# Kernel optimization log

Hardware: AMD Instinct MI355X
Metric: run time of the kernel (lower is better)

The kernel has to match this reference:

```python
import jax, jax.numpy as jnp
import numpy as np

B, NQ, NKV, DQ, DIN = 8, 2048, 2048, 512, 512


def setup_inputs() -> dict:
    key = jax.random.key(0)
    ks = jax.random.split(key, 5)
    scale = 1.0 / np.sqrt(DQ)
    return {
        "query": jax.random.normal(ks[0], (B, NQ, DQ), dtype=jnp.float32),
        "key": jax.random.normal(ks[1], (NKV, DQ), dtype=jnp.float32),
        "x": jax.random.normal(ks[2], (B, NKV, DIN), dtype=jnp.float32),
        "W_proj": jax.random.normal(ks[3], (DQ, DQ), dtype=jnp.float32) * scale,
        "b_proj": jnp.zeros((DQ,), dtype=jnp.float32),
        "W_px": jax.random.normal(ks[4], (DQ, DIN), dtype=jnp.float32) * scale,
        "b_px": jnp.zeros((DQ,), dtype=jnp.float32),
    }


def reference(query, key, x, W_proj, b_proj, W_px, b_px):
    # query_proj = Linear(dim_query, dim_query)(query)            [B, Nq, DQ]
    query_proj = jnp.einsum("bqd,ed->bqe", query, W_proj) + b_proj
    # k = project_x(x) + key.unsqueeze(0)                          [B, Nkv, DQ]
    k = jnp.einsum("bki,ei->bke", x, W_px) + b_px + key[None, :, :]
    # score = bmm(query_proj, k^T)                                 [B, Nq, Nkv]
    score = jnp.einsum("bqe,bke->bqk", query_proj, k)
    # softmax=True branch (note: original applies NO 1/sqrt(d) scaling)
    attn = jax.nn.softmax(score, axis=-1)
    # out = bmm(attn, x)                                           [B, Nq, DIN]
    out = jnp.einsum("bqk,bki->bqi", attn, x)
    return out, attn
```

## Files before the change

kernel.cpp:

```cpp
#include <hip/hip_runtime.h>
#include <hip/hip_bf16.h>

#define B_   8
#define NQ_  2048
#define NKV_ 2048
#define DQ_  512
#define DIN_ 512

using f32x4 = __attribute__((ext_vector_type(4))) float;
using f16   = _Float16;
using f16x4 = __attribute__((ext_vector_type(4))) _Float16;
using f16x8 = __attribute__((ext_vector_type(8))) _Float16;

__device__ __forceinline__ f32x4 mfma16f(f16x8 a, f16x8 b, f32x4 c) {
  return __builtin_amdgcn_mfma_f32_16x16x32_f16(a, b, c, 0, 0, 0);
}

__device__ __forceinline__ void gload_lds16(const void* g, void* l) {
  __builtin_amdgcn_global_load_lds(
      (const __attribute__((address_space(1))) void*)g,
      (__attribute__((address_space(3))) void*)l, 16, 0, 0);
}

__device__ __forceinline__ int xcd_swz(int bid, int nwg) {
  const int c = nwg >> 3;
  return (bid & 7) * c + (bid >> 3);
}

__global__ __launch_bounds__(256, 2)
void proj_gemm(const float* __restrict__ query, const float* __restrict__ W_proj,
               const float* __restrict__ b_proj, f16* __restrict__ qp,
               const float* __restrict__ x, const float* __restrict__ W_px,
               const float* __restrict__ b_px, const float* __restrict__ keyp,
               f16* __restrict__ km, f16* __restrict__ xTp)
{
  constexpr int PAD = 8;
  __shared__ f16 Ah[128][64 + PAD];
  __shared__ f16 Bh[128][64 + PAD];

  const bool second = (blockIdx.z == 1);
  const float* A    = second ? x    : query;
  const float* Bm   = second ? W_px : W_proj;
  const float* bias = second ? b_px : b_proj;
  f16*         C    = second ? km   : qp;

  const int tid  = threadIdx.x;
  const int lane = tid & 63;
  const int w    = tid >> 6;
  const int wr   = w >> 1;
  const int wc   = w & 1;
  const int brow = blockIdx.y * 128;
  const int bcol = blockIdx.x * 128;

  const float* Ag = A  + (size_t)brow * DQ_;
  const float* Bg = Bm + (size_t)bcol * DQ_;

  f32x4 acc[4][4] = {};

  const int sr = tid >> 4;
  const int sc = (tid & 15) * 4;

  float4 pa[8], pb[8];
#pragma unroll
  for (int p = 0; p < 8; ++p) {
    pa[p] = *(const float4*)(Ag + (size_t)(p * 16 + sr) * DQ_ + sc);
    pb[p] = *(const float4*)(Bg + (size_t)(p * 16 + sr) * DQ_ + sc);
  }

  const bool emitXT = second && (blockIdx.x == 0);

  for (int k0 = 0; k0 < DQ_; k0 += 64) {
    __syncthreads();
#pragma unroll
    for (int p = 0; p < 8; ++p) {
      const int r = p * 16 + sr;
      f16x4 ha, hb;
      ha[0] = (f16)pa[p].x; ha[1] = (f16)pa[p].y;
      ha[2] = (f16)pa[p].z; ha[3] = (f16)pa[p].w;
      hb[0] = (f16)pb[p].x; hb[1] = (f16)pb[p].y;
      hb[2] = (f16)pb[p].z; hb[3] = (f16)pb[p].w;
      *(f16x4*)&Ah[r][sc] = ha;
      *(f16x4*)&Bh[r][sc] = hb;
    }
    if (k0 + 64 < DQ_) {
#pragma unroll
      for (int p = 0; p < 8; ++p) {
        pa[p] = *(const float4*)(Ag + (size_t)(p * 16 + sr) * DQ_ + k0 + 64 + sc);
        pb[p] = *(const float4*)(Bg + (size_t)(p * 16 + sr) * DQ_ + k0 + 64 + sc);
      }
    }
    __syncthreads();
#pragma unroll
    for (int kk = 0; kk < 2; ++kk) {
      const int fr = lane & 15;
      const int fc = kk * 32 + (lane >> 4) * 8;
      f16x8 ah[4], bh[4];
#pragma unroll
      for (int m = 0; m < 4; ++m)
        ah[m] = *(const f16x8*)&Ah[wr * 64 + m * 16 + fr][fc];
#pragma unroll
      for (int n = 0; n < 4; ++n)
        bh[n] = *(const f16x8*)&Bh[wc * 64 + n * 16 + fr][fc];
#pragma unroll
      for (int m = 0; m < 4; ++m)
#pragma unroll
        for (int n = 0; n < 4; ++n)
          acc[m][n] = mfma16f(ah[m], bh[n], acc[m][n]);
    }

    if (emitXT) {
      const int dl = tid >> 2;
      const int j0 = (tid & 3) * 32;
      f16* dst = xTp + ((size_t)(brow >> 11) * DIN_ + k0 + dl) * NKV_
                     + (brow & (NKV_ - 1)) + j0;
#pragma unroll
      for (int v = 0; v < 4; ++v) {
        f16x8 tv;
#pragma unroll
        for (int e = 0; e < 8; ++e) tv[e] = Ah[j0 + v * 8 + e][dl];
        *(f16x8*)(dst + v * 8) = tv;
      }
    }
  }

#pragma unroll
  for (int m = 0; m < 4; ++m)
#pragma unroll
    for (int n = 0; n < 4; ++n)
#pragma unroll
      for (int r = 0; r < 4; ++r) {
        const int row_g = brow + wr * 64 + m * 16 + (lane >> 4) * 4 + r;
        const int col_g = bcol + wc * 64 + n * 16 + (lane & 15);
        float vv = acc[m][n][r] + bias[col_g];
        if (second) vv += keyp[(size_t)(row_g & (NKV_ - 1)) * DQ_ + col_g];
        C[(size_t)row_g * DQ_ + col_g] = (f16)vv;
      }
}

__global__ __launch_bounds__(512, 2)
void score_gemm(const f16* __restrict__ qp, const f16* __restrict__ km,
                float* __restrict__ attn)
{
  __shared__ f16 ABuf[2 * 8192];
  __shared__ f16 BBuf[2 * 8192];

  const int swz  = xcd_swz(blockIdx.x, gridDim.x);
  const int bx   = swz & 7;
  const int by   = (swz >> 3) & 7;
  const int b    = swz >> 6;

  const int t    = threadIdx.x;
  const int lane = t & 63;
  const int w    = t >> 6;
  const int wr   = w >> 2;
  const int wcn  = w & 3;
  const int brow = by * 256;
  const int bcol = bx * 256;
  const int fr   = lane & 15;
  const int q    = lane >> 4;
  const int slotE = ((q ^ (fr & 3)) * 8);

  const int srow = t >> 2;
  const int sig  = (t & 3) ^ (srow & 3);
  const f16* aG = qp + ((size_t)b * NQ_  + brow + srow) * DQ_ + sig * 8;
  const f16* bG = km + ((size_t)b * NKV_ + bcol + srow) * DQ_ + sig * 8;

#define STAGE_A(kc) do { \
    const f16* s_ = aG + (kc) * 32; \
    f16* d_ = ABuf + ((kc) & 1) * 8192 + w * 512; \
    gload_lds16(s_, d_); \
    gload_lds16(s_ + (size_t)128 * DQ_, d_ + 4096); } while (0)
#define STAGE_B(kc) do { \
    const f16* s_ = bG + (kc) * 32; \
    f16* d_ = BBuf + ((kc) & 1) * 8192 + w * 512; \
    gload_lds16(s_, d_); \
    gload_lds16(s_ + (size_t)128 * DQ_, d_ + 4096); } while (0)

  f32x4 acc[8][4] = {};

  STAGE_A(0); STAGE_B(0);
  asm volatile("s_waitcnt vmcnt(0)\n\ts_barrier" ::: "memory");

  for (int c = 0; c < 16; ++c) {
    if (c + 1 < 16) { STAGE_A(c + 1); STAGE_B(c + 1); }

    const f16* Ab = ABuf + (c & 1) * 8192;
    const f16* Bb = BBuf + (c & 1) * 8192;

    f16x8 bh[4];
#pragma unroll
    for (int ni = 0; ni < 4; ++ni)
      bh[ni] = *(const f16x8*)&Bb[(wcn * 64 + ni * 16 + fr) * 32 + slotE];

    __builtin_amdgcn_s_setprio(1);
#pragma unroll
    for (int mi = 0; mi < 8; ++mi) {
      const f16x8 ah = *(const f16x8*)&Ab[(wr * 128 + mi * 16 + fr) * 32 + slotE];
#pragma unroll
      for (int ni = 0; ni < 4; ++ni)
        acc[mi][ni] = mfma16f(ah, bh[ni], acc[mi][ni]);
    }
    __builtin_amdgcn_s_setprio(0);

    if (c + 1 < 16)
      asm volatile("s_waitcnt vmcnt(0)\n\ts_barrier" ::: "memory");
  }
#undef STAGE_A
#undef STAGE_B

  float* Cg = attn + (size_t)b * NQ_ * NKV_;
#pragma unroll
  for (int mi = 0; mi < 8; ++mi)
#pragma unroll
    for (int ni = 0; ni < 4; ++ni)
#pragma unroll
      for (int r = 0; r < 4; ++r) {
        const int row_g = brow + wr * 128 + mi * 16 + q * 4 + r;
        const int col_g = bcol + wcn * 64 + ni * 16 + fr;
        Cg[(size_t)row_g * NKV_ + col_g] = acc[mi][ni][r];
      }
}

__global__ __launch_bounds__(256, 2)
void pv_gemm(const f16* __restrict__ attnb, const f16* __restrict__ xT,
             float* __restrict__ out)
{
  __shared__ f16 At[2][128 * 64];
  __shared__ f16 Bt[2][128 * 64];

  const int swz  = xcd_swz(blockIdx.x, gridDim.x);
  const int bx   = swz & 3;
  const int by   = (swz >> 2) & 15;
  const int b    = swz >> 6;

  const int t    = threadIdx.x;
  const int lane = t & 63;
  const int w    = t >> 6;
  const int wr   = w >> 1;
  const int wc   = w & 1;
  const int brow = by * 128;
  const int bcol = bx * 128;

  const int srow  = t >> 3;
  const int sslot = t & 7;
  const int sig   = sslot ^ (srow & 7);
  const f16* aG = attnb + ((size_t)b * NQ_ + brow + srow) * NKV_ + sig * 8;
  const f16* bG = xT + (size_t)b * DIN_ * NKV_ + (size_t)(bcol + srow) * NKV_ + sig * 8;

  f32x4 acc[4][4] = {};
  const int fr = lane & 15;
  const int q  = lane >> 4;

#define PV_STAGE(ks, buf) do { \
    const f16* a_ = aG + (size_t)(ks) * 64; \
    const f16* b_ = bG + (size_t)(ks) * 64; \
    f16* al_ = At[buf] + w * 512; \
    f16* bl_ = Bt[buf] + w * 512; \
    _Pragma("unroll") for (int i = 0; i < 4; ++i) { \
      gload_lds16(a_ + (size_t)i * 32 * NKV_, al_ + i * 2048); \
      gload_lds16(b_ + (size_t)i * 32 * NKV_, bl_ + i * 2048); } } while (0)

  PV_STAGE(0, 0);
  asm volatile("s_waitcnt vmcnt(0)\n\ts_barrier" ::: "memory");

  for (int ks = 0; ks < NKV_ / 64; ++ks) {
    const int cur = ks & 1;
    if (ks + 1 < NKV_ / 64) PV_STAGE(ks + 1, cur ^ 1);

    const f16* Ac = At[cur];
    const f16* Bc = Bt[cur];
#pragma unroll
    for (int kk = 0; kk < 2; ++kk) {
      f16x8 ah[4], bh[4];
#pragma unroll
      for (int m = 0; m < 4; ++m) {
        const int rt = wr * 64 + m * 16 + fr;
        ah[m] = *(const f16x8*)&Ac[rt * 64 + (((kk * 4 + q) ^ (rt & 7)) * 8)];
      }
#pragma unroll
      for (int n = 0; n < 4; ++n) {
        const int rt = wc * 64 + n * 16 + fr;
        bh[n] = *(const f16x8*)&Bc[rt * 64 + (((kk * 4 + q) ^ (rt & 7)) * 8)];
      }
#pragma unroll
      for (int m = 0; m < 4; ++m)
#pragma unroll
        for (int n = 0; n < 4; ++n)
          acc[m][n] = mfma16f(ah[m], bh[n], acc[m][n]);
    }
    asm volatile("s_waitcnt vmcnt(0)\n\ts_barrier" ::: "memory");
  }
#undef PV_STAGE

  float* Cg = out + (size_t)b * NQ_ * DIN_;
#pragma unroll
  for (int m = 0; m < 4; ++m)
#pragma unroll
    for (int n = 0; n < 4; ++n)
#pragma unroll
      for (int r = 0; r < 4; ++r) {
        const int row_g = brow + wr * 64 + m * 16 + q * 4 + r;
        const int col_g = bcol + wc * 64 + n * 16 + fr;
        Cg[(size_t)row_g * DIN_ + col_g] = acc[m][n][r];
      }
}

__global__ void softmax_rows(float* __restrict__ attn, f16* __restrict__ attnb)
{
  const int lane = threadIdx.x & 63;
  const int wv   = threadIdx.x >> 6;
  const size_t row = (size_t)blockIdx.x * 4 + wv;
  float* p  = attn  + row * NKV_;
  f16*   pb = attnb + row * NKV_;

  float4 v[8];
  float mx = -1e30f;
#pragma unroll
  for (int i = 0; i < 8; ++i) {
    v[i] = *(const float4*)&p[i * 256 + lane * 4];
    mx = fmaxf(mx, fmaxf(fmaxf(v[i].x, v[i].y), fmaxf(v[i].z, v[i].w)));
  }
#pragma unroll
  for (int off = 32; off; off >>= 1) mx = fmaxf(mx, __shfl_xor(mx, off, 64));

  float sum = 0.f;
#pragma unroll
  for (int i = 0; i < 8; ++i) {
    v[i].x = expf(v[i].x - mx);
    v[i].y = expf(v[i].y - mx);
    v[i].z = expf(v[i].z - mx);
    v[i].w = expf(v[i].w - mx);
    sum += v[i].x + v[i].y + v[i].z + v[i].w;
  }
#pragma unroll
  for (int off = 32; off; off >>= 1) sum += __shfl_xor(sum, off, 64);

  const float inv = 1.0f / sum;
#pragma unroll
  for (int i = 0; i < 8; ++i) {
    v[i].x *= inv; v[i].y *= inv; v[i].z *= inv; v[i].w *= inv;
    *(float4*)&p[i * 256 + lane * 4] = v[i];
    f16x4 hv;
    hv[0] = (f16)v[i].x; hv[1] = (f16)v[i].y;
    hv[2] = (f16)v[i].z; hv[3] = (f16)v[i].w;
    *(f16x4*)&pb[i * 256 + lane * 4] = hv;
  }
}

extern "C" void kernel_launch(void* const* d_in, const int* in_sizes, int n_in,
                              void* d_out, int out_size, void* d_ws, size_t ws_size,
                              hipStream_t stream)
{
  (void)in_sizes; (void)n_in; (void)out_size; (void)ws_size;
  const float* query  = (const float*)d_in[0];
  const float* key    = (const float*)d_in[1];
  const float* x      = (const float*)d_in[2];
  const float* W_proj = (const float*)d_in[3];
  const float* b_proj = (const float*)d_in[4];
  const float* W_px   = (const float*)d_in[5];
  const float* b_px   = (const float*)d_in[6];

  float* out  = (float*)d_out;
  float* attn = out + (size_t)B_ * NQ_ * DIN_;

  const size_t PQE = (size_t)B_ * NQ_ * DQ_;
  f16* xT = (f16*)d_ws;
  f16* qp = xT + PQE;
  f16* km = qp + PQE;
  f16* attnb = qp;

  proj_gemm<<<dim3(DQ_ / 128, (B_ * NQ_) / 128, 2), 256, 0, stream>>>(
      query, W_proj, b_proj, qp, x, W_px, b_px, key, km, xT);

  score_gemm<<<(NKV_ / 256) * (NQ_ / 256) * B_, 512, 0, stream>>>(qp, km, attn);

  softmax_rows<<<(B_ * NQ_) / 4, 256, 0, stream>>>(attn, attnb);

  pv_gemm<<<(DIN_ / 128) * (NQ_ / 128) * B_, 256, 0, stream>>>(attnb, xT, out);
}
```

Baseline: 227.4 us.

## Fuse softmax into score and PV GEMMs via partial row statistics

```diff
diff --git a/kernel.cpp b/kernel.cpp
--- a/kernel.cpp
+++ b/kernel.cpp
@@ -137,9 +137,9 @@
       }
 }
 
-__global__ __launch_bounds__(512, 2)
+__global__ __launch_bounds__(512, 4)
 void score_gemm(const f16* __restrict__ qp, const f16* __restrict__ km,
-                float* __restrict__ attn)
+                float* __restrict__ rawp, float2* __restrict__ stats)
 {
   __shared__ f16 ABuf[2 * 8192];
   __shared__ f16 BBuf[2 * 8192];
@@ -208,7 +208,25 @@
 #undef STAGE_A
 #undef STAGE_B
 
-  float* Cg = attn + (size_t)b * NQ_ * NKV_;
+  float* Cg = rawp + (size_t)b * NQ_ * NKV_;
+#pragma unroll
+  for (int mi = 0; mi < 8; ++mi)
+#pragma unroll
+    for (int r = 0; r < 4; ++r) {
+      float m = fmaxf(fmaxf(acc[mi][0][r], acc[mi][1][r]),
+                      fmaxf(acc[mi][2][r], acc[mi][3][r]));
+#pragma unroll
+      for (int off = 8; off; off >>= 1) m = fmaxf(m, __shfl_xor(m, off, 64));
+      float s = __expf(acc[mi][0][r] - m) + __expf(acc[mi][1][r] - m)
+              + __expf(acc[mi][2][r] - m) + __expf(acc[mi][3][r] - m);
+#pragma unroll
+      for (int off = 8; off; off >>= 1) s += __shfl_xor(s, off, 64);
+      if (fr == 0) {
+        const size_t R = (size_t)b * NQ_ + brow + wr * 128 + mi * 16 + q * 4 + r;
+        stats[(R << 5) + bx * 4 + wcn] = make_float2(m, s);
+      }
+    }
+
 #pragma unroll
   for (int mi = 0; mi < 8; ++mi)
 #pragma unroll
@@ -221,9 +239,27 @@
       }
 }
 
+__global__ void stats_reduce(const float2* __restrict__ stats,
+                             float2* __restrict__ rowstats)
+{
+  const int R = blockIdx.x * 256 + threadIdx.x;
+  float2 v[32];
+  float m = -1e30f;
+#pragma unroll
+  for (int i = 0; i < 32; ++i) {
+    v[i] = stats[((size_t)R << 5) + i];
+    m = fmaxf(m, v[i].x);
+  }
+  float s = 0.f;
+#pragma unroll
+  for (int i = 0; i < 32; ++i) s += v[i].y * __expf(v[i].x - m);
+  rowstats[R] = make_float2(m, 1.0f / s);
+}
+
 __global__ __launch_bounds__(256, 2)
-void pv_gemm(const f16* __restrict__ attnb, const f16* __restrict__ xT,
-             float* __restrict__ out)
+void pv_gemm(const float* __restrict__ raw, const float2* __restrict__ rowstats,
+             const f16* __restrict__ xT, float* __restrict__ out,
+             float* __restrict__ attn_out)
 {
   __shared__ f16 At[2][128 * 64];
   __shared__ f16 Bt[2][128 * 64];
@@ -240,32 +276,55 @@
   const int wc   = w & 1;
   const int brow = by * 128;
   const int bcol = bx * 128;
-
-  const int srow  = t >> 3;
-  const int sslot = t & 7;
-  const int sig   = sslot ^ (srow & 7);
-  const f16* aG = attnb + ((size_t)b * NQ_ + brow + srow) * NKV_ + sig * 8;
-  const f16* bG = xT + (size_t)b * DIN_ * NKV_ + (size_t)(bcol + srow) * NKV_ + sig * 8;
+  const int fr   = lane & 15;
+  const int q    = lane >> 4;
+
+  const int srow = t >> 3;
+  const int sigB = (t & 7) ^ (srow & 7);
+  const f16* bG = xT + (size_t)b * DIN_ * NKV_ + (size_t)(bcol + srow) * NKV_ + sigB * 8;
+
+  const int c4 = t & 15;
+  const int r0 = t >> 4;
+  const size_t Rbase = (size_t)b * NQ_ + brow;
+  const float* aB = raw + (Rbase + r0) * NKV_ + c4 * 4;
+  float*       nB = attn_out + (Rbase + r0) * NKV_ + c4 * 4;
+  float2 rs[8];
+#pragma unroll
+  for (int j = 0; j < 8; ++j) rs[j] = rowstats[Rbase + r0 + j * 16];
+
+  const bool wrN = (attn_out != nullptr) && (bx == 0);
+
+  float4 av[8];
+#define PV_LOADA(kc) do { \
+    _Pragma("unroll") for (int j = 0; j < 8; ++j) \
+      av[j] = *(const float4*)(aB + (size_t)j * 16 * NKV_ + (kc) * 64); } while (0)
+#define PV_STAGEB(kc, buf) do { \
+    const f16* b_ = bG + (size_t)(kc) * 64; \
+    f16* bl_ = Bt[buf] + w * 512; \
+    _Pragma("unroll") for (int i = 0; i < 4; ++i) \
+      gload_lds16(b_ + (size_t)i * 32 * NKV_, bl_ + i * 2048); } while (0)
+#define PV_PROCA(kc, buf) do { \
+    _Pragma("unroll") for (int j = 0; j < 8; ++j) { \
+      const int rj = r0 + j * 16; \
+      float4 n_; \
+      n_.x = __expf(av[j].x - rs[j].x) * rs[j].y; \
+      n_.y = __expf(av[j].y - rs[j].x) * rs[j].y; \
+      n_.z = __expf(av[j].z - rs[j].x) * rs[j].y; \
+      n_.w = __expf(av[j].w - rs[j].x) * rs[j].y; \
+      if (wrN) *(float4*)(nB + (size_t)j * 16 * NKV_ + (kc) * 64) = n_; \
+      f16x4 hv; hv[0] = (f16)n_.x; hv[1] = (f16)n_.y; \
+      hv[2] = (f16)n_.z; hv[3] = (f16)n_.w; \
+      *(f16x4*)&At[buf][rj * 64 + (((c4 >> 1) ^ (rj & 7)) * 8) + (c4 & 1) * 4] = hv; \
+    } } while (0)
 
   f32x4 acc[4][4] = {};
-  const int fr = lane & 15;
-  const int q  = lane >> 4;
-
-#define PV_STAGE(ks, buf) do { \
-    const f16* a_ = aG + (size_t)(ks) * 64; \
-    const f16* b_ = bG + (size_t)(ks) * 64; \
-    f16* al_ = At[buf] + w * 512; \
-    f16* bl_ = Bt[buf] + w * 512; \
-    _Pragma("unroll") for (int i = 0; i < 4; ++i) { \
-      gload_lds16(a_ + (size_t)i * 32 * NKV_, al_ + i * 2048); \
-      gload_lds16(b_ + (size_t)i * 32 * NKV_, bl_ + i * 2048); } } while (0)
-
-  PV_STAGE(0, 0);
-  asm volatile("s_waitcnt vmcnt(0)\n\ts_barrier" ::: "memory");
+
+  PV_LOADA(0); PV_STAGEB(0, 0); PV_PROCA(0, 0);
+  __syncthreads();
 
   for (int ks = 0; ks < NKV_ / 64; ++ks) {
     const int cur = ks & 1;
-    if (ks + 1 < NKV_ / 64) PV_STAGE(ks + 1, cur ^ 1);
+    if (ks + 1 < NKV_ / 64) { PV_LOADA(ks + 1); PV_STAGEB(ks + 1, cur ^ 1); }
 
     const f16* Ac = At[cur];
     const f16* Bc = Bt[cur];
@@ -282,15 +341,20 @@
         const int rt = wc * 64 + n * 16 + fr;
         bh[n] = *(const f16x8*)&Bc[rt * 64 + (((kk * 4 + q) ^ (rt & 7)) * 8)];
       }
+      __builtin_amdgcn_s_setprio(1);
 #pragma unroll
       for (int m = 0; m < 4; ++m)
 #pragma unroll
         for (int n = 0; n < 4; ++n)
           acc[m][n] = mfma16f(ah[m], bh[n], acc[m][n]);
-    }
-    asm volatile("s_waitcnt vmcnt(0)\n\ts_barrier" ::: "memory");
+      __builtin_amdgcn_s_setprio(0);
+    }
+    if (ks + 1 < NKV_ / 64) PV_PROCA(ks + 1, cur ^ 1);
+    __syncthreads();
   }
-#undef PV_STAGE
+#undef PV_LOADA
+#undef PV_STAGEB
+#undef PV_PROCA
 
   float* Cg = out + (size_t)b * NQ_ * DIN_;
 #pragma unroll
@@ -305,53 +369,25 @@
       }
 }
 
-__global__ void softmax_rows(float* __restrict__ attn, f16* __restrict__ attnb)
-{
-  const int lane = threadIdx.x & 63;
-  const int wv   = threadIdx.x >> 6;
-  const size_t row = (size_t)blockIdx.x * 4 + wv;
-  float* p  = attn  + row * NKV_;
-  f16*   pb = attnb + row * NKV_;
-
-  float4 v[8];
-  float mx = -1e30f;
-#pragma unroll
-  for (int i = 0; i < 8; ++i) {
-    v[i] = *(const float4*)&p[i * 256 + lane * 4];
-    mx = fmaxf(mx, fmaxf(fmaxf(v[i].x, v[i].y), fmaxf(v[i].z, v[i].w)));
-  }
-#pragma unroll
-  for (int off = 32; off; off >>= 1) mx = fmaxf(mx, __shfl_xor(mx, off, 64));
-
-  float sum = 0.f;
-#pragma unroll
-  for (int i = 0; i < 8; ++i) {
-    v[i].x = expf(v[i].x - mx);
-    v[i].y = expf(v[i].y - mx);
-    v[i].z = expf(v[i].z - mx);
-    v[i].w = expf(v[i].w - mx);
-    sum += v[i].x + v[i].y + v[i].z + v[i].w;
-  }
-#pragma unroll
-  for (int off = 32; off; off >>= 1) sum += __shfl_xor(sum, off, 64);
-
-  const float inv = 1.0f / sum;
-#pragma unroll
-  for (int i = 0; i < 8; ++i) {
-    v[i].x *= inv; v[i].y *= inv; v[i].z *= inv; v[i].w *= inv;
-    *(float4*)&p[i * 256 + lane * 4] = v[i];
-    f16x4 hv;
-    hv[0] = (f16)v[i].x; hv[1] = (f16)v[i].y;
-    hv[2] = (f16)v[i].z; hv[3] = (f16)v[i].w;
-    *(f16x4*)&pb[i * 256 + lane * 4] = hv;
-  }
+__global__ void normalize_attn(float* __restrict__ attn,
+                               const float2* __restrict__ rowstats)
+{
+  const size_t i4 = (size_t)blockIdx.x * 256 + threadIdx.x;
+  const int R = (int)(i4 >> 9);
+  const float2 rs = rowstats[R];
+  float4 v = ((const float4*)attn)[i4];
+  v.x = __expf(v.x - rs.x) * rs.y;
+  v.y = __expf(v.y - rs.x) * rs.y;
+  v.z = __expf(v.z - rs.x) * rs.y;
+  v.w = __expf(v.w - rs.x) * rs.y;
+  ((float4*)attn)[i4] = v;
 }
 
 extern "C" void kernel_launch(void* const* d_in, const int* in_sizes, int n_in,
                               void* d_out, int out_size, void* d_ws, size_t ws_size,
                               hipStream_t stream)
 {
-  (void)in_sizes; (void)n_in; (void)out_size; (void)ws_size;
+  (void)in_sizes; (void)n_in; (void)out_size;
   const float* query  = (const float*)d_in[0];
   const float* key    = (const float*)d_in[1];
   const float* x      = (const float*)d_in[2];
@@ -363,18 +399,34 @@
   float* out  = (float*)d_out;
   float* attn = out + (size_t)B_ * NQ_ * DIN_;
 
-  const size_t PQE = (size_t)B_ * NQ_ * DQ_;
-  f16* xT = (f16*)d_ws;
-  f16* qp = xT + PQE;
-  f16* km = qp + PQE;
-  f16* attnb = qp;
+  const size_t PQE  = (size_t)B_ * NQ_ * DQ_;
+  const size_t ROWS = (size_t)B_ * NQ_;
+
+  f16*    xT       = (f16*)d_ws;
+  f16*    qp       = xT + PQE;
+  f16*    km       = qp + PQE;
+  float2* stats    = (float2*)(km + PQE);
+  float2* rowstats = stats + ROWS * 32;
+  float*  rawws    = (float*)(rowstats + ROWS);
+
+  const size_t need = (size_t)((char*)(rawws + ROWS * NKV_) - (char*)d_ws);
+  const bool big = (ws_size >= need);
+
+  float* rawp     = big ? rawws : attn;
+  float* attn_out = big ? attn  : nullptr;
 
   proj_gemm<<<dim3(DQ_ / 128, (B_ * NQ_) / 128, 2), 256, 0, stream>>>(
       query, W_proj, b_proj, qp, x, W_px, b_px, key, km, xT);
 
-  score_gemm<<<(NKV_ / 256) * (NQ_ / 256) * B_, 512, 0, stream>>>(qp, km, attn);
-
-  softmax_rows<<<(B_ * NQ_) / 4, 256, 0, stream>>>(attn, attnb);
-
-  pv_gemm<<<(DIN_ / 128) * (NQ_ / 128) * B_, 256, 0, stream>>>(attnb, xT, out);
-}
+  score_gemm<<<(NKV_ / 256) * (NQ_ / 256) * B_, 512, 0, stream>>>(
+      qp, km, rawp, stats);
+
+  stats_reduce<<<(int)(ROWS / 256), 256, 0, stream>>>(stats, rowstats);
+
+  pv_gemm<<<(DIN_ / 128) * (NQ_ / 128) * B_, 256, 0, stream>>>(
+      rawp, rowstats, xT, out, attn_out);
+
+  if (!big)
+    normalize_attn<<<(int)(ROWS * NKV_ / 4 / 256), 256, 0, stream>>>(
+        attn, rowstats);
+}
```

Measured after the change: 420.2 us. 1.85x slower.
